# Kernel tuning notes

Measured on AMD Instinct MI355X. Metric: run time of the kernel, lower is better.

Reference implementation:

```python
import jax, jax.numpy as jnp
import numpy as np

HEADS = 4
KS = 7  # neighborhood window size


def group_norm(x, g, b, eps=1e-5):
    # GroupNorm(1, C) on NCHW: normalize over (C,H,W) per sample
    mu = x.mean(axis=(1, 2, 3), keepdims=True)
    var = x.var(axis=(1, 2, 3), keepdims=True)
    xn = (x - mu) * jax.lax.rsqrt(var + eps)
    return xn * g[None, :, None, None] + b[None, :, None, None]


def layer_norm(x, g, b, eps=1e-5):
    mu = x.mean(axis=-1, keepdims=True)
    var = x.var(axis=-1, keepdims=True)
    return (x - mu) * jax.lax.rsqrt(var + eps) * g + b


def na2d(x, qkv_w, qkv_b, proj_w, proj_b, rpb):
    # Neighborhood attention 2D (NATTEN semantics: window clamped at borders)
    N, H, W, C = x.shape
    e, k = HEADS, KS
    d = C // e
    qkv = x @ qkv_w.T + qkv_b  # [N,H,W,3C]
    q, kk, v = jnp.split(qkv, 3, axis=-1)
    q = q.reshape(N, H, W, e, d) * (d ** -0.5)
    kk = kk.reshape(N, H, W, e, d)
    v = v.reshape(N, H, W, e, d)
    ni = jnp.clip(jnp.arange(H) - k // 2, 0, H - k)[:, None] + jnp.arange(k)  # [H,k]
    nj = jnp.clip(jnp.arange(W) - k // 2, 0, W - k)[:, None] + jnp.arange(k)  # [W,k]
    kg = kk[:, ni][:, :, :, nj]  # [N,H,i,W,j,e,d]
    vg = v[:, ni][:, :, :, nj]
    scores = jnp.einsum('nhwed,nhiwjed->nhweij', q, kg)  # [N,H,W,e,k,k]
    ri = ni - jnp.arange(H)[:, None] + (k - 1)  # rel pos index in [0, 2k-2]
    rj = nj - jnp.arange(W)[:, None] + (k - 1)
    bias = rpb[:, ri][:, :, :, rj]  # [e,H,i,W,j]
    scores = scores + bias.transpose(1, 3, 0, 2, 4)[None]
    attn = jax.nn.softmax(scores.reshape(N, H, W, e, k * k), axis=-1).reshape(N, H, W, e, k, k)
    out = jnp.einsum('nhweij,nhiwjed->nhwed', attn, vg).reshape(N, H, W, C)
    return out @ proj_w.T + proj_b


def na_layer(x, gn_g, gn_b, qkv_w, qkv_b, proj_w, proj_b, rpb, ln_g, ln_b, fc1_w, fc1_b, fc2_w, fc2_b):
    N, C, H, W = x.shape
    x1 = x.transpose(0, 2, 3, 1)  # n h w c (pre-norm residual)
    xg = group_norm(x, gn_g, gn_b).transpose(0, 2, 3, 1)
    a = na2d(xg, qkv_w, qkv_b, proj_w, proj_b, rpb) + x1
    t = a.reshape(N, H * W, C)
    h = jax.nn.gelu(layer_norm(t, ln_g, ln_b) @ fc1_w.T + fc1_b, approximate=False)
    t = t + (h @ fc2_w.T + fc2_b)
    return t.reshape(N, H, W, C).transpose(0, 3, 1, 2)


def conv3x3(x, w, b):
    y = jax.lax.conv_general_dilated(x, w, (1, 1), 'SAME', dimension_numbers=('NCHW', 'OIHW', 'NCHW'))
    return y + b[None, :, None, None]


def setup_inputs() -> dict:
    key = jax.random.key(0)
    ks = jax.random.split(key, 16)
    N, C, H, W = 2, 128, 64, 64
    L, e, k, hid, red = 2, HEADS, KS, 4 * 128, 18
    rn = lambda kk, shape, s=0.02: jax.random.normal(kk, shape, jnp.float32) * s
    return {
        'x': jax.random.normal(ks[0], (N, C, H, W), jnp.float32),
        'gn_g': jnp.ones((L, C), jnp.float32), 'gn_b': jnp.zeros((L, C), jnp.float32),
        'qkv_w': rn(ks[1], (L, 3 * C, C)), 'qkv_b': jnp.zeros((L, 3 * C), jnp.float32),
        'proj_w': rn(ks[2], (L, C, C)), 'proj_b': jnp.zeros((L, C), jnp.float32),
        'rpb': rn(ks[3], (L, e, 2 * k - 1, 2 * k - 1)),
        'ln_g': jnp.ones((L, C), jnp.float32), 'ln_b': jnp.zeros((L, C), jnp.float32),
        'fc1_w': rn(ks[4], (L, hid, C)), 'fc1_b': jnp.zeros((L, hid), jnp.float32),
        'fc2_w': rn(ks[5], (L, C, hid)), 'fc2_b': jnp.zeros((L, C), jnp.float32),
        'bconv_w': rn(ks[6], (C, C, 3, 3)), 'bconv_b': jnp.zeros((C,), jnp.float32),
        'c1_w': rn(ks[7], (C // 4, C)), 'c1_b': jnp.zeros((C // 4,), jnp.float32),
        'c2_w': rn(ks[8], (C, C // 4)), 'c2_b': jnp.zeros((C,), jnp.float32),
        'ca1_w': rn(ks[9], (C // red, C)), 'ca1_b': jnp.zeros((C // red,), jnp.float32),
        'ca2_w': rn(ks[10], (C, C // red)), 'ca2_b': jnp.zeros((C,), jnp.float32),
    }


def reference(x, gn_g, gn_b, qkv_w, qkv_b, proj_w, proj_b, rpb, ln_g, ln_b, fc1_w, fc1_b, fc2_w, fc2_b, bconv_w, bconv_b, c1_w, c1_b, c2_w, c2_b, ca1_w, ca1_b, ca2_w, ca2_b):
    res = x
    for l in range(gn_g.shape[0]):  # n_resblocks (structurally fixed, small)
        res = na_layer(res, gn_g[l], gn_b[l], qkv_w[l], qkv_b[l], proj_w[l], proj_b[l], rpb[l],
                       ln_g[l], ln_b[l], fc1_w[l], fc1_b[l], fc2_w[l], fc2_b[l])
    res = conv3x3(res, bconv_w, bconv_b)
    # tail: 1x1 conv -> ReLU -> 1x1 conv -> CALayer
    y = jax.nn.relu(jnp.einsum('rc,nchw->nrhw', c1_w, res) + c1_b[None, :, None, None])
    y = jnp.einsum('cr,nrhw->nchw', c2_w, y) + c2_b[None, :, None, None]
    p = y.mean(axis=(2, 3))  # global avg pool -> [N,C]
    s = jax.nn.sigmoid(jax.nn.relu(p @ ca1_w.T + ca1_b) @ ca2_w.T + ca2_b)
    y = y * s[:, :, None, None]
    return y + x
```

## Files before the change

### kernel.cpp

```cpp
#include <hip/hip_runtime.h>
#include <math.h>

typedef unsigned short u16;

#define NN 2
#define CC 128
#define HH 64
#define WW 64
#define NHD 4
#define DH 32
#define KSZ 7
#define NB 49
#define PIX (NN*HH*WW)
#define HID 512
#define C4 32
#define CRED 7
#define RW 22
#define RNB 160
#define NBV 154

typedef float f32x4 __attribute__((ext_vector_type(4)));
typedef short bf16x8 __attribute__((ext_vector_type(8)));

static __device__ __forceinline__ float u2f(u16 u){ return __uint_as_float(((unsigned)u) << 16); }
static __device__ __forceinline__ u16 f2u(float f){
    unsigned b = __float_as_uint(f);
    return (u16)((b + 0x7FFFu + ((b >> 16) & 1u)) >> 16);
}

__global__ void detect_k(const u16* __restrict__ x, int* __restrict__ flag,
                         float* __restrict__ poolacc){
    __shared__ float red[256];
    int t = threadIdx.x;
    float mx = 0.f;
    for(int i = t; i < 4096; i += 256){
        float v = fabsf(u2f(x[i]));
        if(v < 1e30f) mx = fmaxf(mx, v);
    }
    red[t] = mx; __syncthreads();
    for(int s = 128; s > 0; s >>= 1){
        if(t < s) red[t] = fmaxf(red[t], red[t+s]);
        __syncthreads();
    }
    if(t == 0) *flag = (red[0] > 1e6f) ? 1 : 0;
    if(t < NN*CC) poolacc[t] = 0.f;
}

struct PtrTab { const void* p[23]; int off[24]; };

__global__ void cvt_all_k(PtrTab tab, u16* __restrict__ dst, const int* __restrict__ flag, int total){
    int i = blockIdx.x*256 + threadIdx.x;
    if(i >= total) return;
    int a = 0;
    while(i >= tab.off[a+1]) a++;
    int loc = i - tab.off[a];
    dst[i] = (*flag) ? f2u(((const float*)tab.p[a])[loc]) : ((const u16*)tab.p[a])[loc];
}

__global__ void repack_conv_k(const u16* __restrict__ src, u16* __restrict__ dst){
    int i = blockIdx.x*256 + threadIdx.x;
    if(i >= CC*CC*9) return;
    int o = i/(9*CC); int rem = i%(9*CC); int tap = rem/CC; int c = rem%CC;
    dst[i] = src[(o*CC + c)*9 + tap];
}

__global__ __launch_bounds__(256) void nchw_k(const void* __restrict__ x, float* __restrict__ cur,
                                              float* __restrict__ part, const int* __restrict__ flag){
    __shared__ float tile[32][65];
    __shared__ float wred[4][2];
    int bx = blockIdx.x;
    int by = blockIdx.y;
    int n = by >> 6, i = by & 63;
    int t = threadIdx.x;
    int fl = *flag;
    for(int idx = t; idx < 32*64; idx += 256){
        int cl = idx >> 6, j = idx & 63;
        size_t src = ((size_t)(n*CC + bx*32 + cl)*HH + i)*WW + j;
        tile[cl][j] = fl ? ((const float*)x)[src] : u2f(((const u16*)x)[src]);
    }
    __syncthreads();
    float s = 0.f, q = 0.f;
    for(int idx = t; idx < 64*32; idx += 256){
        int j = idx >> 5, cl = idx & 31;
        float v = tile[cl][j];
        cur[((size_t)((n*HH + i)*WW) + j)*CC + bx*32 + cl] = v;
        s += v; q += v*v;
    }
    #pragma unroll
    for(int off = 32; off > 0; off >>= 1){ s += __shfl_xor(s, off, 64); q += __shfl_xor(q, off, 64); }
    int wave = t >> 6;
    if((t & 63) == 0){ wred[wave][0] = s; wred[wave][1] = q; }
    __syncthreads();
    if(t == 0){
        float ss = wred[0][0]+wred[1][0]+wred[2][0]+wred[3][0];
        float qq = wred[0][1]+wred[1][1]+wred[2][1]+wred[3][1];
        int pidx = n*256 + (by & 63)*4 + bx;
        part[pidx*2] = ss; part[pidx*2+1] = qq;
    }
}

__global__ void gn_r2_k(const float* __restrict__ part, float* __restrict__ stats, int count){
    __shared__ float s1[256]; __shared__ float s2[256];
    int n = blockIdx.x, t = threadIdx.x;
    float a = 0.f, q = 0.f;
    for(int idx = t; idx < count; idx += 256){
        a += part[(n*count + idx)*2];
        q += part[(n*count + idx)*2 + 1];
    }
    s1[t] = a; s2[t] = q; __syncthreads();
    for(int s = 128; s > 0; s >>= 1){
        if(t < s){ s1[t] += s1[t+s]; s2[t] += s2[t+s]; }
        __syncthreads();
    }
    if(t == 0){
        const float inv = 1.f/(float)(HH*WW*CC);
        float mu = s1[0]*inv;
        float var = fmaxf(s2[0]*inv - mu*mu, 0.f);
        stats[n*2] = mu; stats[n*2+1] = rsqrtf(var + 1e-5f);
    }
}

enum { EPI_NONE = 0, EPI_RES = 1, EPI_GELU = 2, EPI_RELU = 3 };
enum { OUT_F32 = 0, OUT_BF16 = 1, OUT_BOTH = 2 };
enum { EX_NONE = 0, EX_STATS = 1, EX_POOL = 2 };

template<int BK, int EPI, int OUTM, int AGN, int EXTRA>
__global__ __launch_bounds__(256) void g64_k(
    const void* __restrict__ Av, const u16* __restrict__ W, const u16* __restrict__ bias,
    const float* __restrict__ R, float* __restrict__ Cf, u16* __restrict__ Cb,
    const float* __restrict__ stats, const u16* __restrict__ gnw, const u16* __restrict__ gnb,
    float* __restrict__ gnpart, float* __restrict__ poolacc,
    int M, int N, int K)
{
    const int LDP = BK + 8;
    const int CH  = BK/8;
    const int NL  = (64*CH)/256;
    __shared__ __align__(16) u16 As[64*(BK+8)];
    __shared__ __align__(16) u16 Bs[64*(BK+8)];
    __shared__ float wred[4][2];
    const int bm = blockIdx.y*64, bn = blockIdx.x*64;
    const int t = threadIdx.x;
    const int wave = t >> 6, lane = t & 63;
    const int wm = (wave >> 1)*32, wn = (wave & 1)*32;
    const int lg = lane >> 4, lr = lane & 15;
    const int nsm = bm >> 12;
    f32x4 acc[2][2];
    #pragma unroll
    for(int i = 0; i < 2; i++)
        #pragma unroll
        for(int j = 0; j < 2; j++) acc[i][j] = (f32x4){0.f,0.f,0.f,0.f};

    float gmu = 0.f, grs = 0.f;
    if(AGN){ gmu = stats[nsm*2]; grs = stats[nsm*2+1]; }

    for(int k0 = 0; k0 < K; k0 += BK){
        uint4 ra[NL], rb[NL];
        float4 fa[NL][2];
        #pragma unroll
        for(int r = 0; r < NL; r++){
            int e = r*256 + t;
            int row = e / CH, ch = e % CH;
            if(AGN){
                const float* ap = (const float*)Av + (size_t)(bm+row)*K + k0 + ch*8;
                fa[r][0] = *(const float4*)ap;
                fa[r][1] = *(const float4*)(ap + 4);
            } else {
                ra[r] = *(const uint4*)((const u16*)Av + (size_t)(bm+row)*K + k0 + ch*8);
            }
            rb[r] = (bn+row < N) ? *(const uint4*)(W + (size_t)(bn+row)*K + k0 + ch*8)
                                 : (uint4){0,0,0,0};
        }
        #pragma unroll
        for(int r = 0; r < NL; r++){
            int e = r*256 + t;
            int row = e / CH, ch = e % CH;
            if(AGN){
                union { uint4 u; u16 h[8]; } g8, b8, o8;
                g8.u = *(const uint4*)(gnw + k0 + ch*8);
                b8.u = *(const uint4*)(gnb + k0 + ch*8);
                const float* fv = (const float*)&fa[r][0];
                #pragma unroll
                for(int z = 0; z < 8; z++)
                    o8.h[z] = f2u((fv[z]-gmu)*grs*u2f(g8.h[z]) + u2f(b8.h[z]));
                *(uint4*)&As[row*LDP + ch*8] = o8.u;
            } else {
                *(uint4*)&As[row*LDP + ch*8] = ra[r];
            }
            *(uint4*)&Bs[row*LDP + ch*8] = rb[r];
        }
        __syncthreads();
        #pragma unroll
        for(int kc = 0; kc < BK/32; kc++){
            bf16x8 af0 = *(const bf16x8*)&As[(wm + lr)*LDP      + kc*32 + lg*8];
            bf16x8 af1 = *(const bf16x8*)&As[(wm + 16 + lr)*LDP + kc*32 + lg*8];
            bf16x8 bf0 = *(const bf16x8*)&Bs[(wn + lr)*LDP      + kc*32 + lg*8];
            bf16x8 bf1 = *(const bf16x8*)&Bs[(wn + 16 + lr)*LDP + kc*32 + lg*8];
            acc[0][0] = __builtin_amdgcn_mfma_f32_16x16x32_bf16(af0, bf0, acc[0][0], 0, 0, 0);
            acc[0][1] = __builtin_amdgcn_mfma_f32_16x16x32_bf16(af0, bf1, acc[0][1], 0, 0, 0);
            acc[1][0] = __builtin_amdgcn_mfma_f32_16x16x32_bf16(af1, bf0, acc[1][0], 0, 0, 0);
            acc[1][1] = __builtin_amdgcn_mfma_f32_16x16x32_bf16(af1, bf1, acc[1][1], 0, 0, 0);
        }
        __syncthreads();
    }

    float ssum = 0.f, sq = 0.f;
    float cs[2] = {0.f, 0.f};
    #pragma unroll
    for(int i = 0; i < 2; i++){
        #pragma unroll
        for(int j = 0; j < 2; j++){
            int col = bn + wn + j*16 + lr;
            if(col >= N) continue;
            #pragma unroll
            for(int reg = 0; reg < 4; reg++){
                int row = bm + wm + i*16 + lg*4 + reg;
                float v = acc[i][j][reg] + u2f(bias[col]);
                if(EPI == EPI_RES)  v += R[(size_t)row*N + col];
                if(EPI == EPI_GELU) v = 0.5f*v*(1.f + erff(v*0.70710678118f));
                if(EPI == EPI_RELU) v = fmaxf(v, 0.f);
                if(OUTM == OUT_F32 || OUTM == OUT_BOTH) Cf[(size_t)row*N + col] = v;
                if(OUTM == OUT_BF16 || OUTM == OUT_BOTH) Cb[(size_t)row*N + col] = f2u(v);
                if(EXTRA == EX_STATS){ ssum += v; sq += v*v; }
                if(EXTRA == EX_POOL) cs[j] += v;
            }
        }
    }
    if(EXTRA == EX_STATS){
        #pragma unroll
        for(int off = 32; off > 0; off >>= 1){
            ssum += __shfl_xor(ssum, off, 64); sq += __shfl_xor(sq, off, 64);
        }
        if(lane == 0){ wred[wave][0] = ssum; wred[wave][1] = sq; }
        __syncthreads();
        if(t == 0){
            int bidx = blockIdx.y*gridDim.x + blockIdx.x;
            gnpart[bidx*2]   = wred[0][0]+wred[1][0]+wred[2][0]+wred[3][0];
            gnpart[bidx*2+1] = wred[0][1]+wred[1][1]+wred[2][1]+wred[3][1];
        }
    }
    if(EXTRA == EX_POOL){
        #pragma unroll
        for(int j = 0; j < 2; j++){
            cs[j] += __shfl_xor(cs[j], 16, 64);
            cs[j] += __shfl_xor(cs[j], 32, 64);
        }
        if(lg == 0){
            #pragma unroll
            for(int j = 0; j < 2; j++){
                int col = bn + wn + j*16 + lr;
                if(col < N) atomicAdd(&poolacc[nsm*CC + col], cs[j]);
            }
        }
    }
}

__global__ __launch_bounds__(256) void mconv_k(
    const u16* __restrict__ in, const u16* __restrict__ Wt,
    const u16* __restrict__ bias, u16* __restrict__ Cb)
{
    const int LDP = 72;
    __shared__ __align__(16) u16 As[64*72];
    __shared__ __align__(16) u16 Bs[64*72];
    const int bm = blockIdx.y*64, bn = blockIdx.x*64;
    const int t = threadIdx.x;
    const int wave = t >> 6, lane = t & 63;
    const int wm = (wave >> 1)*32, wn = (wave & 1)*32;
    const int lg = lane >> 4, lr = lane & 15;
    f32x4 acc[2][2];
    #pragma unroll
    for(int i = 0; i < 2; i++)
        #pragma unroll
        for(int j = 0; j < 2; j++) acc[i][j] = (f32x4){0.f,0.f,0.f,0.f};

    for(int k0 = 0; k0 < 9*CC; k0 += 64){
        int tap = k0 >> 7; int dy = tap/3 - 1, dx = tap%3 - 1;
        int coff = k0 & 127;
        uint4 ra[2], rb[2];
        #pragma unroll
        for(int r = 0; r < 2; r++){
            int e = r*256 + t;
            int row = e >> 3, ch = e & 7;
            int p = bm + row;
            int n = p >> 12, ii = (p & 4095) >> 6, jj = p & 63;
            int y = ii + dy, x = jj + dx;
            ra[r] = (uint4){0,0,0,0};
            if(y >= 0 && y < HH && x >= 0 && x < WW)
                ra[r] = *(const uint4*)(in + (size_t)(((n*HH + y)*WW + x))*CC + coff + ch*8);
            rb[r] = *(const uint4*)(Wt + (size_t)(bn+row)*(9*CC) + k0 + ch*8);
        }
        #pragma unroll
        for(int r = 0; r < 2; r++){
            int e = r*256 + t;
            int row = e >> 3, ch = e & 7;
            *(uint4*)&As[row*LDP + ch*8] = ra[r];
            *(uint4*)&Bs[row*LDP + ch*8] = rb[r];
        }
        __syncthreads();
        #pragma unroll
        for(int kc = 0; kc < 2; kc++){
            bf16x8 af0 = *(const bf16x8*)&As[(wm + lr)*LDP      + kc*32 + lg*8];
            bf16x8 af1 = *(const bf16x8*)&As[(wm + 16 + lr)*LDP + kc*32 + lg*8];
            bf16x8 bf0 = *(const bf16x8*)&Bs[(wn + lr)*LDP      + kc*32 + lg*8];
            bf16x8 bf1 = *(const bf16x8*)&Bs[(wn + 16 + lr)*LDP + kc*32 + lg*8];
            acc[0][0] = __builtin_amdgcn_mfma_f32_16x16x32_bf16(af0, bf0, acc[0][0], 0, 0, 0);
            acc[0][1] = __builtin_amdgcn_mfma_f32_16x16x32_bf16(af0, bf1, acc[0][1], 0, 0, 0);
            acc[1][0] = __builtin_amdgcn_mfma_f32_16x16x32_bf16(af1, bf0, acc[1][0], 0, 0, 0);
            acc[1][1] = __builtin_amdgcn_mfma_f32_16x16x32_bf16(af1, bf1, acc[1][1], 0, 0, 0);
        }
        __syncthreads();
    }
    #pragma unroll
    for(int i = 0; i < 2; i++){
        #pragma unroll
        for(int j = 0; j < 2; j++){
            int col = bn + wn + j*16 + lr;
            #pragma unroll
            for(int reg = 0; reg < 4; reg++){
                int row = bm + wm + i*16 + lg*4 + reg;
                Cb[(size_t)row*CC + col] = f2u(acc[i][j][reg] + u2f(bias[col]));
            }
        }
    }
}

#define KVP 72
#define PSP 168

__global__ __launch_bounds__(128) void att_tile_k(
    const u16* __restrict__ qkv, const u16* __restrict__ rpb, u16* __restrict__ out)
{
    __shared__ __align__(16) u16 KV[2][RNB][KVP];
    __shared__ __align__(16) u16 Qs[16][64];
    __shared__ __align__(16) u16 Ps[2][16][PSP];
    __shared__ float rpbs[2][169];
    const int blk = blockIdx.x;
    const int rb = blk >> 1, eg = blk & 1;
    const int p0 = rb*16;
    const int jb = p0 & 63, i = (p0 >> 6) & 63, n = p0 >> 12;
    const int i0 = min(max(i-3, 0), HH-KSZ);
    const int rc0 = min(max(jb-3, 0), WW-KSZ);
    const int t = threadIdx.x;

    for(int idx = t; idx < 2*169; idx += 128)
        rpbs[idx/169][idx%169] = u2f(rpb[(eg*2 + idx/169)*169 + idx%169]);
    {
        int pix = t >> 3, ch = t & 7;
        *(uint4*)&Qs[pix][ch*8] = *(const uint4*)(qkv + (size_t)(p0+pix)*(3*CC) + eg*64 + ch*8);
    }
    for(int idx = t; idx < RNB*16; idx += 128){
        int nb = idx >> 4, part = idx & 15;
        int kv = part >> 3, ch = part & 7;
        uint4 v = (uint4){0,0,0,0};
        if(nb < NBV){
            int ky = nb/RW, kcol = nb - ky*RW;
            int sy = i0 + ky, sx = min(rc0 + kcol, WW-1);
            v = *(const uint4*)(qkv + (size_t)((n*HH + sy)*WW + sx)*(3*CC) + CC + kv*CC + eg*64 + ch*8);
        }
        *(uint4*)&KV[kv][nb][ch*8] = v;
    }
    __syncthreads();

    const int el = t >> 6;
    const int lane = t & 63, lg = lane >> 4, lr = lane & 15;

    bf16x8 aq = *(const bf16x8*)&Qs[lr][el*32 + lg*8];
    f32x4 sc[10];
    #pragma unroll
    for(int c = 0; c < 10; c++){
        bf16x8 bk = *(const bf16x8*)&KV[0][c*16+lr][el*32 + lg*8];
        sc[c] = __builtin_amdgcn_mfma_f32_16x16x32_bf16(aq, bk, (f32x4){0.f,0.f,0.f,0.f}, 0, 0, 0);
    }
    #pragma unroll
    for(int reg = 0; reg < 4; reg++){
        int pix = lg*4 + reg;
        int j = jb + pix;
        int base = min(max(j-3, 0), WW-KSZ) - rc0;
        float mx = -1e30f;
        #pragma unroll
        for(int c = 0; c < 10; c++){
            int nb = c*16 + lr;
            int ky = nb/RW, kcol = nb - ky*RW;
            float v = -1e30f;
            if(nb < NBV && kcol >= base && kcol <= base+6){
                int ri = i0 + ky - i + (KSZ-1);
                int rj = rc0 + kcol - j + (KSZ-1);
                v = sc[c][reg]*0.17677669529663689f + rpbs[el][ri*13 + rj];
            }
            sc[c][reg] = v;
            mx = fmaxf(mx, v);
        }
        mx = fmaxf(mx, __shfl_xor(mx, 1, 64));
        mx = fmaxf(mx, __shfl_xor(mx, 2, 64));
        mx = fmaxf(mx, __shfl_xor(mx, 4, 64));
        mx = fmaxf(mx, __shfl_xor(mx, 8, 64));
        float sum = 0.f;
        #pragma unroll
        for(int c = 0; c < 10; c++){
            float p = __expf(sc[c][reg] - mx);
            sc[c][reg] = p; sum += p;
        }
        sum += __shfl_xor(sum, 1, 64);
        sum += __shfl_xor(sum, 2, 64);
        sum += __shfl_xor(sum, 4, 64);
        sum += __shfl_xor(sum, 8, 64);
        float rs = 1.f/sum;
        #pragma unroll
        for(int c = 0; c < 10; c++)
            Ps[el][pix][c*16+lr] = f2u(sc[c][reg]*rs);
    }
    __syncthreads();
    f32x4 o0 = (f32x4){0.f,0.f,0.f,0.f}, o1 = (f32x4){0.f,0.f,0.f,0.f};
    #pragma unroll
    for(int ks = 0; ks < 5; ks++){
        bf16x8 ap = *(const bf16x8*)&Ps[el][lr][ks*32 + lg*8];
        bf16x8 b0, b1;
        #pragma unroll
        for(int jj = 0; jj < 8; jj++){
            int nb = ks*32 + lg*8 + jj;
            b0[jj] = (short)KV[1][nb][el*32 + lr];
            b1[jj] = (short)KV[1][nb][el*32 + 16 + lr];
        }
        o0 = __builtin_amdgcn_mfma_f32_16x16x32_bf16(ap, b0, o0, 0, 0, 0);
        o1 = __builtin_amdgcn_mfma_f32_16x16x32_bf16(ap, b1, o1, 0, 0, 0);
    }
    int e = eg*2 + el;
    #pragma unroll
    for(int reg = 0; reg < 4; reg++){
        int pix = lg*4 + reg;
        out[(size_t)(p0+pix)*CC + e*32 + lr]      = f2u(o0[reg]);
        out[(size_t)(p0+pix)*CC + e*32 + 16 + lr] = f2u(o1[reg]);
    }
}

__global__ void ln_k(const float* __restrict__ a, const u16* __restrict__ g,
                     const u16* __restrict__ b, u16* __restrict__ out){
    int wave = threadIdx.x >> 6;
    int lane = threadIdx.x & 63;
    int p = blockIdx.x*4 + wave;
    if(p >= PIX) return;
    const float* row = a + (size_t)p*CC;
    float v1 = row[lane], v2 = row[lane+64];
    float s = v1 + v2, q = v1*v1 + v2*v2;
    #pragma unroll
    for(int off = 32; off > 0; off >>= 1){
        s += __shfl_xor(s, off, 64);
        q += __shfl_xor(q, off, 64);
    }
    float mu = s*(1.f/CC);
    float rstd = rsqrtf(fmaxf(q*(1.f/CC) - mu*mu, 0.f) + 1e-5f);
    u16* o = out + (size_t)p*CC;
    o[lane]    = f2u((v1-mu)*rstd*u2f(g[lane])    + u2f(b[lane]));
    o[lane+64] = f2u((v2-mu)*rstd*u2f(g[lane+64]) + u2f(b[lane+64]));
}

__global__ void ca_k(const float* __restrict__ poolacc,
                     const u16* __restrict__ w1, const u16* __restrict__ b1,
                     const u16* __restrict__ w2, const u16* __restrict__ b2,
                     float* __restrict__ s){
    __shared__ float pl[CC]; __shared__ float t1[CRED];
    int n = blockIdx.x, t = threadIdx.x;
    pl[t] = poolacc[n*CC + t]*(1.f/(HH*WW));
    __syncthreads();
    if(t < CRED){
        float a = u2f(b1[t]);
        for(int c = 0; c < CC; c++) a += pl[c]*u2f(w1[t*CC + c]);
        t1[t] = fmaxf(a, 0.f);
    }
    __syncthreads();
    float a = u2f(b2[t]);
    #pragma unroll
    for(int r = 0; r < CRED; r++) a += t1[r]*u2f(w2[t*CRED + r]);
    s[n*CC + t] = 1.f/(1.f + __expf(-a));
}

__global__ void final_k(const float* __restrict__ y, const float* __restrict__ s,
                        const void* __restrict__ xraw, void* __restrict__ outv,
                        const int* __restrict__ flag){
    int id = blockIdx.x*256 + threadIdx.x;
    if(id >= NN*CC*HH*WW) return;
    int j = id % WW; int i = (id/WW) % HH; int c = (id/(WW*HH)) % CC; int n = id/(WW*HH*CC);
    float xr = (*flag) ? ((const float*)xraw)[id] : u2f(((const u16*)xraw)[id]);
    float v = y[(size_t)((n*HH + i)*WW + j)*CC + c]*s[n*CC + c] + xr;
    if(*flag) ((float*)outv)[id] = v;
    else      ((u16*)outv)[id] = f2u(v);
}

extern "C" void kernel_launch(void* const* d_in, const int* in_sizes, int n_in,
                              void* d_out, int out_size, void* d_ws, size_t ws_size,
                              hipStream_t stream){
    float* wsf    = (float*)d_ws;
    int*   flagp  = (int*)d_ws;
    float* stats  = wsf + 4;
    float* gnpart = wsf + 8;
    float* poolacc= wsf + 1040;
    float* sbuf   = wsf + 1300;

    u16* Wb = (u16*)(wsf + 2048);
    static const int wsizes[23] = {256,256,98304,768,32768,256,1352,256,256,131072,1024,
                                   131072,256,147456,128,4096,32,4096,128,896,7,896,128};
    int woff[24]; woff[0] = 0;
    for(int i = 0; i < 23; i++) woff[i+1] = woff[i] + wsizes[i];
    const int WTOT = woff[23];
    u16* Wt = Wb + 555760;

    float* AB    = wsf + 360448;
    float* cur   = AB;
    u16*  cur16  = (u16*)(AB + 1048576);
    u16*  xg16   = (u16*)(AB + 1572864);
    u16*  qkv16  = (u16*)(AB + 2097152);
    float* abuf  = AB + 2097152;
    u16*  hbuf16 = (u16*)(AB + 3670016);
    float* ybuf  = AB + 3670016;
    u16*  y1     = (u16*)(AB + 4718592);

    detect_k<<<1, 256, 0, stream>>>((const u16*)d_in[0], flagp, poolacc);

    PtrTab tab;
    for(int i = 0; i < 23; i++){ tab.p[i] = d_in[i+1]; tab.off[i] = woff[i]; }
    tab.off[23] = woff[23];
    cvt_all_k<<<(WTOT + 255)/256, 256, 0, stream>>>(tab, Wb, flagp, WTOT);
    repack_conv_k<<<(CC*CC*9 + 255)/256, 256, 0, stream>>>(Wb + woff[13], Wt);

    const u16 *gng = Wb+woff[0], *gnb = Wb+woff[1], *qkvw = Wb+woff[2], *qkvb = Wb+woff[3],
              *projw = Wb+woff[4], *projb = Wb+woff[5], *rpbw = Wb+woff[6], *lng = Wb+woff[7],
              *lnb = Wb+woff[8], *f1w = Wb+woff[9], *f1b = Wb+woff[10], *f2w = Wb+woff[11],
              *f2b = Wb+woff[12], *bcb = Wb+woff[14], *c1w = Wb+woff[15],
              *c1b = Wb+woff[16], *c2w = Wb+woff[17], *c2b = Wb+woff[18], *ca1w = Wb+woff[19],
              *ca1b = Wb+woff[20], *ca2w = Wb+woff[21], *ca2b = Wb+woff[22];

    nchw_k<<<dim3(4, NN*HH), 256, 0, stream>>>(d_in[0], cur, gnpart, flagp);

    for(int l = 0; l < 2; l++){
        gn_r2_k<<<NN, 256, 0, stream>>>(gnpart, stats, l == 0 ? 256 : 128);

        g64_k<64,EPI_NONE,OUT_BF16,1,EX_NONE><<<dim3(6, PIX/64), 256, 0, stream>>>(
            cur, qkvw + (size_t)l*3*CC*CC, qkvb + l*3*CC, nullptr, nullptr, qkv16,
            stats, gng + l*CC, gnb + l*CC, nullptr, nullptr, PIX, 3*CC, CC);

        att_tile_k<<<PIX/16*2, 128, 0, stream>>>(qkv16, rpbw + l*NHD*169, xg16);

        g64_k<64,EPI_RES,OUT_F32,0,EX_NONE><<<dim3(2, PIX/64), 256, 0, stream>>>(
            xg16, projw + (size_t)l*CC*CC, projb + l*CC, cur, abuf, nullptr,
            nullptr, nullptr, nullptr, nullptr, nullptr, PIX, CC, CC);

        ln_k<<<PIX/4, 256, 0, stream>>>(abuf, lng + l*CC, lnb + l*CC, xg16);

        g64_k<64,EPI_GELU,OUT_BF16,0,EX_NONE><<<dim3(8, PIX/64), 256, 0, stream>>>(
            xg16, f1w + (size_t)l*HID*CC, f1b + l*HID, nullptr, nullptr, hbuf16,
            nullptr, nullptr, nullptr, nullptr, nullptr, PIX, HID, CC);

        g64_k<64,EPI_RES,OUT_BOTH,0,EX_STATS><<<dim3(2, PIX/64), 256, 0, stream>>>(
            hbuf16, f2w + (size_t)l*CC*HID, f2b + l*CC, abuf, cur, cur16,
            nullptr, nullptr, nullptr, gnpart, nullptr, PIX, CC, HID);
    }

    mconv_k<<<dim3(2, PIX/64), 256, 0, stream>>>(cur16, Wt, bcb, xg16);

    g64_k<64,EPI_RELU,OUT_BF16,0,EX_NONE><<<dim3(1, PIX/64), 256, 0, stream>>>(
        xg16, c1w, c1b, nullptr, nullptr, y1,
        nullptr, nullptr, nullptr, nullptr, nullptr, PIX, C4, CC);

    g64_k<32,EPI_NONE,OUT_F32,0,EX_POOL><<<dim3(2, PIX/64), 256, 0, stream>>>(
        y1, c2w, c2b, nullptr, ybuf, nullptr,
        nullptr, nullptr, nullptr, nullptr, poolacc, PIX, CC, C4);

    ca_k<<<NN, CC, 0, stream>>>(poolacc, ca1w, ca1b, ca2w, ca2b, sbuf);
    final_k<<<(NN*CC*HH*WW)/256, 256, 0, stream>>>(ybuf, sbuf, d_in[0], d_out, flagp);
}
```

Baseline: 298.6 us.

## Fuse setup, GN stats, proj+LayerNorm, tail GEMMs and CA into fewer kernels

```diff
diff --git a/kernel.cpp b/kernel.cpp
--- a/kernel.cpp
+++ b/kernel.cpp
@@ -10,7 +10,6 @@
 #define NHD 4
 #define DH 32
 #define KSZ 7
-#define NB 49
 #define PIX (NN*HH*WW)
 #define HID 512
 #define C4 32
@@ -47,32 +46,43 @@
 }
 
 struct PtrTab { const void* p[23]; int off[24]; };
-
-__global__ void cvt_all_k(PtrTab tab, u16* __restrict__ dst, const int* __restrict__ flag, int total){
-    int i = blockIdx.x*256 + threadIdx.x;
-    if(i >= total) return;
-    int a = 0;
-    while(i >= tab.off[a+1]) a++;
-    int loc = i - tab.off[a];
-    dst[i] = (*flag) ? f2u(((const float*)tab.p[a])[loc]) : ((const u16*)tab.p[a])[loc];
-}
-
-__global__ void repack_conv_k(const u16* __restrict__ src, u16* __restrict__ dst){
-    int i = blockIdx.x*256 + threadIdx.x;
-    if(i >= CC*CC*9) return;
-    int o = i/(9*CC); int rem = i%(9*CC); int tap = rem/CC; int c = rem%CC;
-    dst[i] = src[(o*CC + c)*9 + tap];
-}
-
-__global__ __launch_bounds__(256) void nchw_k(const void* __restrict__ x, float* __restrict__ cur,
-                                              float* __restrict__ part, const int* __restrict__ flag){
+#define NCVT 2172
+#define NRPK 576
+#define NNCH 512
+
+__global__ __launch_bounds__(256) void setup_k(
+    PtrTab tab, u16* __restrict__ Wb, u16* __restrict__ Wt,
+    const void* __restrict__ convw, const void* __restrict__ x,
+    float* __restrict__ cur, float* __restrict__ part,
+    const int* __restrict__ flag, int total)
+{
+    int blk = blockIdx.x;
+    int t = threadIdx.x;
+    int fl = *flag;
+    if(blk < NCVT){
+        int i = blk*256 + t;
+        if(i < total){
+            int a = 0;
+            while(i >= tab.off[a+1]) a++;
+            int loc = i - tab.off[a];
+            Wb[i] = fl ? f2u(((const float*)tab.p[a])[loc]) : ((const u16*)tab.p[a])[loc];
+        }
+        return;
+    }
+    if(blk < NCVT + NRPK){
+        int i = (blk - NCVT)*256 + t;
+        if(i < CC*CC*9){
+            int o = i/(9*CC); int rem = i%(9*CC); int tap = rem/CC; int c = rem%CC;
+            size_t s = (size_t)(o*CC + c)*9 + tap;
+            Wt[i] = fl ? f2u(((const float*)convw)[s]) : ((const u16*)convw)[s];
+        }
+        return;
+    }
     __shared__ float tile[32][65];
     __shared__ float wred[4][2];
-    int bx = blockIdx.x;
-    int by = blockIdx.y;
+    int u = blk - NCVT - NRPK;
+    int bx = u & 3, by = u >> 2;
     int n = by >> 6, i = by & 63;
-    int t = threadIdx.x;
-    int fl = *flag;
     for(int idx = t; idx < 32*64; idx += 256){
         int cl = idx >> 6, j = idx & 63;
         size_t src = ((size_t)(n*CC + bx*32 + cl)*HH + i)*WW + j;
@@ -94,49 +104,26 @@
     if(t == 0){
         float ss = wred[0][0]+wred[1][0]+wred[2][0]+wred[3][0];
         float qq = wred[0][1]+wred[1][1]+wred[2][1]+wred[3][1];
-        int pidx = n*256 + (by & 63)*4 + bx;
+        int pidx = n*256 + i*4 + bx;
         part[pidx*2] = ss; part[pidx*2+1] = qq;
     }
 }
 
-__global__ void gn_r2_k(const float* __restrict__ part, float* __restrict__ stats, int count){
-    __shared__ float s1[256]; __shared__ float s2[256];
-    int n = blockIdx.x, t = threadIdx.x;
-    float a = 0.f, q = 0.f;
-    for(int idx = t; idx < count; idx += 256){
-        a += part[(n*count + idx)*2];
-        q += part[(n*count + idx)*2 + 1];
-    }
-    s1[t] = a; s2[t] = q; __syncthreads();
-    for(int s = 128; s > 0; s >>= 1){
-        if(t < s){ s1[t] += s1[t+s]; s2[t] += s2[t+s]; }
-        __syncthreads();
-    }
-    if(t == 0){
-        const float inv = 1.f/(float)(HH*WW*CC);
-        float mu = s1[0]*inv;
-        float var = fmaxf(s2[0]*inv - mu*mu, 0.f);
-        stats[n*2] = mu; stats[n*2+1] = rsqrtf(var + 1e-5f);
-    }
-}
-
-enum { EPI_NONE = 0, EPI_RES = 1, EPI_GELU = 2, EPI_RELU = 3 };
+enum { EPI_NONE = 0, EPI_RES = 1, EPI_GELU = 2 };
 enum { OUT_F32 = 0, OUT_BF16 = 1, OUT_BOTH = 2 };
-enum { EX_NONE = 0, EX_STATS = 1, EX_POOL = 2 };
-
-template<int BK, int EPI, int OUTM, int AGN, int EXTRA>
+enum { EX_NONE = 0, EX_STATS = 1 };
+#define LDP 136
+
+template<int EPI, int OUTM, int AGN, int EXTRA>
 __global__ __launch_bounds__(256) void g64_k(
     const void* __restrict__ Av, const u16* __restrict__ W, const u16* __restrict__ bias,
     const float* __restrict__ R, float* __restrict__ Cf, u16* __restrict__ Cb,
-    const float* __restrict__ stats, const u16* __restrict__ gnw, const u16* __restrict__ gnb,
-    float* __restrict__ gnpart, float* __restrict__ poolacc,
+    const u16* __restrict__ gnw, const u16* __restrict__ gnb,
+    float* __restrict__ gnpart, int gncount,
     int M, int N, int K)
 {
-    const int LDP = BK + 8;
-    const int CH  = BK/8;
-    const int NL  = (64*CH)/256;
-    __shared__ __align__(16) u16 As[64*(BK+8)];
-    __shared__ __align__(16) u16 Bs[64*(BK+8)];
+    __shared__ __align__(16) u16 As[64*LDP];
+    __shared__ __align__(16) u16 Bs[64*LDP];
     __shared__ float wred[4][2];
     const int bm = blockIdx.y*64, bn = blockIdx.x*64;
     const int t = threadIdx.x;
@@ -151,15 +138,28 @@
         for(int j = 0; j < 2; j++) acc[i][j] = (f32x4){0.f,0.f,0.f,0.f};
 
     float gmu = 0.f, grs = 0.f;
-    if(AGN){ gmu = stats[nsm*2]; grs = stats[nsm*2+1]; }
-
-    for(int k0 = 0; k0 < K; k0 += BK){
-        uint4 ra[NL], rb[NL];
-        float4 fa[NL][2];
-        #pragma unroll
-        for(int r = 0; r < NL; r++){
+    if(AGN){
+        float a = 0.f, q = 0.f;
+        for(int idx = lane; idx < gncount; idx += 64){
+            a += gnpart[(nsm*gncount + idx)*2];
+            q += gnpart[(nsm*gncount + idx)*2 + 1];
+        }
+        #pragma unroll
+        for(int off = 32; off > 0; off >>= 1){
+            a += __shfl_xor(a, off, 64); q += __shfl_xor(q, off, 64);
+        }
+        const float inv = 1.f/(float)(HH*WW*CC);
+        gmu = a*inv;
+        grs = rsqrtf(fmaxf(q*inv - gmu*gmu, 0.f) + 1e-5f);
+    }
+
+    for(int k0 = 0; k0 < K; k0 += 128){
+        uint4 ra[4], rb[4];
+        float4 fa[4][2];
+        #pragma unroll
+        for(int r = 0; r < 4; r++){
             int e = r*256 + t;
-            int row = e / CH, ch = e % CH;
+            int row = e >> 4, ch = e & 15;
             if(AGN){
                 const float* ap = (const float*)Av + (size_t)(bm+row)*K + k0 + ch*8;
                 fa[r][0] = *(const float4*)ap;
@@ -171,9 +171,9 @@
                                  : (uint4){0,0,0,0};
         }
         #pragma unroll
-        for(int r = 0; r < NL; r++){
+        for(int r = 0; r < 4; r++){
             int e = r*256 + t;
-            int row = e / CH, ch = e % CH;
+            int row = e >> 4, ch = e & 15;
             if(AGN){
                 union { uint4 u; u16 h[8]; } g8, b8, o8;
                 g8.u = *(const uint4*)(gnw + k0 + ch*8);
@@ -190,7 +190,7 @@
         }
         __syncthreads();
         #pragma unroll
-        for(int kc = 0; kc < BK/32; kc++){
+        for(int kc = 0; kc < 4; kc++){
             bf16x8 af0 = *(const bf16x8*)&As[(wm + lr)*LDP      + kc*32 + lg*8];
             bf16x8 af1 = *(const bf16x8*)&As[(wm + 16 + lr)*LDP + kc*32 + lg*8];
             bf16x8 bf0 = *(const bf16x8*)&Bs[(wn + lr)*LDP      + kc*32 + lg*8];
@@ -200,11 +200,10 @@
             acc[1][0] = __builtin_amdgcn_mfma_f32_16x16x32_bf16(af1, bf0, acc[1][0], 0, 0, 0);
             acc[1][1] = __builtin_amdgcn_mfma_f32_16x16x32_bf16(af1, bf1, acc[1][1], 0, 0, 0);
         }
-        __syncthreads();
+        if(k0 + 128 < K) __syncthreads();
     }
 
     float ssum = 0.f, sq = 0.f;
-    float cs[2] = {0.f, 0.f};
     #pragma unroll
     for(int i = 0; i < 2; i++){
         #pragma unroll
@@ -217,11 +216,9 @@
                 float v = acc[i][j][reg] + u2f(bias[col]);
                 if(EPI == EPI_RES)  v += R[(size_t)row*N + col];
                 if(EPI == EPI_GELU) v = 0.5f*v*(1.f + erff(v*0.70710678118f));
-                if(EPI == EPI_RELU) v = fmaxf(v, 0.f);
                 if(OUTM == OUT_F32 || OUTM == OUT_BOTH) Cf[(size_t)row*N + col] = v;
                 if(OUTM == OUT_BF16 || OUTM == OUT_BOTH) Cb[(size_t)row*N + col] = f2u(v);
                 if(EXTRA == EX_STATS){ ssum += v; sq += v*v; }
-                if(EXTRA == EX_POOL) cs[j] += v;
             }
         }
     }
@@ -238,17 +235,106 @@
             gnpart[bidx*2+1] = wred[0][1]+wred[1][1]+wred[2][1]+wred[3][1];
         }
     }
-    if(EXTRA == EX_POOL){
-        #pragma unroll
-        for(int j = 0; j < 2; j++){
-            cs[j] += __shfl_xor(cs[j], 16, 64);
-            cs[j] += __shfl_xor(cs[j], 32, 64);
-        }
-        if(lg == 0){
-            #pragma unroll
-            for(int j = 0; j < 2; j++){
-                int col = bn + wn + j*16 + lr;
-                if(col < N) atomicAdd(&poolacc[nsm*CC + col], cs[j]);
+}
+
+__global__ __launch_bounds__(256) void proj_ln_k(
+    const u16* __restrict__ A, const u16* __restrict__ W, const u16* __restrict__ bias,
+    const float* __restrict__ R, const u16* __restrict__ lng, const u16* __restrict__ lnb,
+    float* __restrict__ abuf, u16* __restrict__ lnout)
+{
+    __shared__ __align__(16) u16 As[64*LDP];
+    __shared__ __align__(16) u16 Bs[128*LDP];
+    __shared__ float redS[64][2], redQ[64][2], muS[64], rsS[64];
+    const int bm = blockIdx.x*64;
+    const int t = threadIdx.x;
+    const int wave = t >> 6, lane = t & 63;
+    const int wm = (wave >> 1)*32, wn = (wave & 1)*64;
+    const int lg = lane >> 4, lr = lane & 15;
+
+    {
+        uint4 ra[4], rb[8];
+        #pragma unroll
+        for(int r = 0; r < 4; r++){
+            int e = r*256 + t; int row = e >> 4, ch = e & 15;
+            ra[r] = *(const uint4*)(A + (size_t)(bm+row)*CC + ch*8);
+        }
+        #pragma unroll
+        for(int r = 0; r < 8; r++){
+            int e = r*256 + t; int row = e >> 4, ch = e & 15;
+            rb[r] = *(const uint4*)(W + (size_t)row*CC + ch*8);
+        }
+        #pragma unroll
+        for(int r = 0; r < 4; r++){
+            int e = r*256 + t; int row = e >> 4, ch = e & 15;
+            *(uint4*)&As[row*LDP + ch*8] = ra[r];
+        }
+        #pragma unroll
+        for(int r = 0; r < 8; r++){
+            int e = r*256 + t; int row = e >> 4, ch = e & 15;
+            *(uint4*)&Bs[row*LDP + ch*8] = rb[r];
+        }
+    }
+    __syncthreads();
+
+    f32x4 acc[2][4];
+    #pragma unroll
+    for(int i = 0; i < 2; i++)
+        #pragma unroll
+        for(int j = 0; j < 4; j++) acc[i][j] = (f32x4){0.f,0.f,0.f,0.f};
+    #pragma unroll
+    for(int kc = 0; kc < 4; kc++){
+        bf16x8 af[2], bf[4];
+        #pragma unroll
+        for(int i = 0; i < 2; i++)
+            af[i] = *(const bf16x8*)&As[(wm + i*16 + lr)*LDP + kc*32 + lg*8];
+        #pragma unroll
+        for(int j = 0; j < 4; j++)
+            bf[j] = *(const bf16x8*)&Bs[(wn + j*16 + lr)*LDP + kc*32 + lg*8];
+        #pragma unroll
+        for(int i = 0; i < 2; i++)
+            #pragma unroll
+            for(int j = 0; j < 4; j++)
+                acc[i][j] = __builtin_amdgcn_mfma_f32_16x16x32_bf16(af[i], bf[j], acc[i][j], 0, 0, 0);
+    }
+    #pragma unroll
+    for(int i = 0; i < 2; i++){
+        #pragma unroll
+        for(int reg = 0; reg < 4; reg++){
+            int rl = wm + i*16 + lg*4 + reg;
+            float rs_ = 0.f, rq_ = 0.f;
+            #pragma unroll
+            for(int j = 0; j < 4; j++){
+                int col = wn + j*16 + lr;
+                float v = acc[i][j][reg] + u2f(bias[col]) + R[(size_t)(bm+rl)*CC + col];
+                acc[i][j][reg] = v;
+                abuf[(size_t)(bm+rl)*CC + col] = v;
+                rs_ += v; rq_ += v*v;
+            }
+            rs_ += __shfl_xor(rs_, 1, 64); rq_ += __shfl_xor(rq_, 1, 64);
+            rs_ += __shfl_xor(rs_, 2, 64); rq_ += __shfl_xor(rq_, 2, 64);
+            rs_ += __shfl_xor(rs_, 4, 64); rq_ += __shfl_xor(rq_, 4, 64);
+            rs_ += __shfl_xor(rs_, 8, 64); rq_ += __shfl_xor(rq_, 8, 64);
+            if(lr == 0){ redS[rl][wn>>6] = rs_; redQ[rl][wn>>6] = rq_; }
+        }
+    }
+    __syncthreads();
+    if(t < 64){
+        float mu = (redS[t][0] + redS[t][1])*(1.f/CC);
+        float var = fmaxf((redQ[t][0] + redQ[t][1])*(1.f/CC) - mu*mu, 0.f);
+        muS[t] = mu; rsS[t] = rsqrtf(var + 1e-5f);
+    }
+    __syncthreads();
+    #pragma unroll
+    for(int i = 0; i < 2; i++){
+        #pragma unroll
+        for(int reg = 0; reg < 4; reg++){
+            int rl = wm + i*16 + lg*4 + reg;
+            float mu = muS[rl], rstd = rsS[rl];
+            #pragma unroll
+            for(int j = 0; j < 4; j++){
+                int col = wn + j*16 + lr;
+                float v = (acc[i][j][reg] - mu)*rstd*u2f(lng[col]) + u2f(lnb[col]);
+                lnout[(size_t)(bm+rl)*CC + col] = f2u(v);
             }
         }
     }
@@ -258,9 +344,8 @@
     const u16* __restrict__ in, const u16* __restrict__ Wt,
     const u16* __restrict__ bias, u16* __restrict__ Cb)
 {
-    const int LDP = 72;
-    __shared__ __align__(16) u16 As[64*72];
-    __shared__ __align__(16) u16 Bs[64*72];
+    __shared__ __align__(16) u16 As[64*LDP];
+    __shared__ __align__(16) u16 Bs[64*LDP];
     const int bm = blockIdx.y*64, bn = blockIdx.x*64;
     const int t = threadIdx.x;
     const int wave = t >> 6, lane = t & 63;
@@ -272,32 +357,32 @@
         #pragma unroll
         for(int j = 0; j < 2; j++) acc[i][j] = (f32x4){0.f,0.f,0.f,0.f};
 
-    for(int k0 = 0; k0 < 9*CC; k0 += 64){
-        int tap = k0 >> 7; int dy = tap/3 - 1, dx = tap%3 - 1;
-        int coff = k0 & 127;
-        uint4 ra[2], rb[2];
-        #pragma unroll
-        for(int r = 0; r < 2; r++){
+    for(int tap = 0; tap < 9; tap++){
+        int dy = tap/3 - 1, dx = tap%3 - 1;
+        int k0 = tap*128;
+        uint4 ra[4], rb[4];
+        #pragma unroll
+        for(int r = 0; r < 4; r++){
             int e = r*256 + t;
-            int row = e >> 3, ch = e & 7;
+            int row = e >> 4, ch = e & 15;
             int p = bm + row;
             int n = p >> 12, ii = (p & 4095) >> 6, jj = p & 63;
             int y = ii + dy, x = jj + dx;
             ra[r] = (uint4){0,0,0,0};
             if(y >= 0 && y < HH && x >= 0 && x < WW)
-                ra[r] = *(const uint4*)(in + (size_t)(((n*HH + y)*WW + x))*CC + coff + ch*8);
+                ra[r] = *(const uint4*)(in + (size_t)(((n*HH + y)*WW + x))*CC + ch*8);
             rb[r] = *(const uint4*)(Wt + (size_t)(bn+row)*(9*CC) + k0 + ch*8);
         }
         #pragma unroll
-        for(int r = 0; r < 2; r++){
+        for(int r = 0; r < 4; r++){
             int e = r*256 + t;
-            int row = e >> 3, ch = e & 7;
+            int row = e >> 4, ch = e & 15;
             *(uint4*)&As[row*LDP + ch*8] = ra[r];
             *(uint4*)&Bs[row*LDP + ch*8] = rb[r];
         }
         __syncthreads();
         #pragma unroll
-        for(int kc = 0; kc < 2; kc++){
+        for(int kc = 0; kc < 4; kc++){
             bf16x8 af0 = *(const bf16x8*)&As[(wm + lr)*LDP      + kc*32 + lg*8];
             bf16x8 af1 = *(const bf16x8*)&As[(wm + 16 + lr)*LDP + kc*32 + lg*8];
             bf16x8 bf0 = *(const bf16x8*)&Bs[(wn + lr)*LDP      + kc*32 + lg*8];
@@ -307,7 +392,7 @@
             acc[1][0] = __builtin_amdgcn_mfma_f32_16x16x32_bf16(af1, bf0, acc[1][0], 0, 0, 0);
             acc[1][1] = __builtin_amdgcn_mfma_f32_16x16x32_bf16(af1, bf1, acc[1][1], 0, 0, 0);
         }
-        __syncthreads();
+        if(tap < 8) __syncthreads();
     }
     #pragma unroll
     for(int i = 0; i < 2; i++){
@@ -432,55 +517,158 @@
     }
 }
 
-__global__ void ln_k(const float* __restrict__ a, const u16* __restrict__ g,
-                     const u16* __restrict__ b, u16* __restrict__ out){
-    int wave = threadIdx.x >> 6;
-    int lane = threadIdx.x & 63;
-    int p = blockIdx.x*4 + wave;
-    if(p >= PIX) return;
-    const float* row = a + (size_t)p*CC;
-    float v1 = row[lane], v2 = row[lane+64];
-    float s = v1 + v2, q = v1*v1 + v2*v2;
-    #pragma unroll
-    for(int off = 32; off > 0; off >>= 1){
-        s += __shfl_xor(s, off, 64);
-        q += __shfl_xor(q, off, 64);
-    }
-    float mu = s*(1.f/CC);
-    float rstd = rsqrtf(fmaxf(q*(1.f/CC) - mu*mu, 0.f) + 1e-5f);
-    u16* o = out + (size_t)p*CC;
-    o[lane]    = f2u((v1-mu)*rstd*u2f(g[lane])    + u2f(b[lane]));
-    o[lane+64] = f2u((v2-mu)*rstd*u2f(g[lane+64]) + u2f(b[lane+64]));
-}
-
-__global__ void ca_k(const float* __restrict__ poolacc,
-                     const u16* __restrict__ w1, const u16* __restrict__ b1,
-                     const u16* __restrict__ w2, const u16* __restrict__ b2,
-                     float* __restrict__ s){
-    __shared__ float pl[CC]; __shared__ float t1[CRED];
-    int n = blockIdx.x, t = threadIdx.x;
-    pl[t] = poolacc[n*CC + t]*(1.f/(HH*WW));
-    __syncthreads();
+__global__ __launch_bounds__(256) void tail_k(
+    const u16* __restrict__ A, const u16* __restrict__ c1w, const u16* __restrict__ c1b,
+    const u16* __restrict__ c2w, const u16* __restrict__ c2b,
+    float* __restrict__ ybuf, float* __restrict__ poolacc)
+{
+    __shared__ __align__(16) u16 As[64*LDP];
+    __shared__ __align__(16) u16 Bs1[32*LDP];
+    __shared__ __align__(16) u16 Hs[64*40];
+    __shared__ __align__(16) u16 Bs2[128*40];
+    const int bm = blockIdx.x*64;
+    const int t = threadIdx.x;
+    const int wave = t >> 6, lane = t & 63;
+    const int lg = lane >> 4, lr = lane & 15;
+    const int nsm = bm >> 12;
+
+    {
+        uint4 ra[4], rb1[2], rb2[2];
+        #pragma unroll
+        for(int r = 0; r < 4; r++){
+            int e = r*256 + t; int row = e >> 4, ch = e & 15;
+            ra[r] = *(const uint4*)(A + (size_t)(bm+row)*CC + ch*8);
+        }
+        #pragma unroll
+        for(int r = 0; r < 2; r++){
+            int e = r*256 + t; int row = e >> 4, ch = e & 15;
+            rb1[r] = *(const uint4*)(c1w + (size_t)row*CC + ch*8);
+        }
+        #pragma unroll
+        for(int r = 0; r < 2; r++){
+            int e = r*256 + t; int row = e >> 2, ch = e & 3;
+            rb2[r] = *(const uint4*)(c2w + (size_t)row*C4 + ch*8);
+        }
+        #pragma unroll
+        for(int r = 0; r < 4; r++){
+            int e = r*256 + t; int row = e >> 4, ch = e & 15;
+            *(uint4*)&As[row*LDP + ch*8] = ra[r];
+        }
+        #pragma unroll
+        for(int r = 0; r < 2; r++){
+            int e = r*256 + t; int row = e >> 4, ch = e & 15;
+            *(uint4*)&Bs1[row*LDP + ch*8] = rb1[r];
+        }
+        #pragma unroll
+        for(int r = 0; r < 2; r++){
+            int e = r*256 + t; int row = e >> 2, ch = e & 3;
+            *(uint4*)&Bs2[row*40 + ch*8] = rb2[r];
+        }
+    }
+    __syncthreads();
+
+    {
+        const int wm1 = (wave >> 1)*32, wn1 = (wave & 1)*16;
+        f32x4 a1[2];
+        a1[0] = (f32x4){0.f,0.f,0.f,0.f}; a1[1] = (f32x4){0.f,0.f,0.f,0.f};
+        #pragma unroll
+        for(int kc = 0; kc < 4; kc++){
+            bf16x8 bf = *(const bf16x8*)&Bs1[(wn1 + lr)*LDP + kc*32 + lg*8];
+            bf16x8 af0 = *(const bf16x8*)&As[(wm1 + lr)*LDP      + kc*32 + lg*8];
+            bf16x8 af1 = *(const bf16x8*)&As[(wm1 + 16 + lr)*LDP + kc*32 + lg*8];
+            a1[0] = __builtin_amdgcn_mfma_f32_16x16x32_bf16(af0, bf, a1[0], 0, 0, 0);
+            a1[1] = __builtin_amdgcn_mfma_f32_16x16x32_bf16(af1, bf, a1[1], 0, 0, 0);
+        }
+        #pragma unroll
+        for(int i = 0; i < 2; i++){
+            #pragma unroll
+            for(int reg = 0; reg < 4; reg++){
+                int rl = wm1 + i*16 + lg*4 + reg;
+                int col = wn1 + lr;
+                Hs[rl*40 + col] = f2u(fmaxf(a1[i][reg] + u2f(c1b[col]), 0.f));
+            }
+        }
+    }
+    __syncthreads();
+
+    {
+        const int wm = (wave >> 1)*32, wn = (wave & 1)*64;
+        f32x4 a2[2][4];
+        #pragma unroll
+        for(int i = 0; i < 2; i++)
+            #pragma unroll
+            for(int j = 0; j < 4; j++) a2[i][j] = (f32x4){0.f,0.f,0.f,0.f};
+        bf16x8 af[2];
+        #pragma unroll
+        for(int i = 0; i < 2; i++)
+            af[i] = *(const bf16x8*)&Hs[(wm + i*16 + lr)*40 + lg*8];
+        #pragma unroll
+        for(int j = 0; j < 4; j++){
+            bf16x8 bf = *(const bf16x8*)&Bs2[(wn + j*16 + lr)*40 + lg*8];
+            a2[0][j] = __builtin_amdgcn_mfma_f32_16x16x32_bf16(af[0], bf, a2[0][j], 0, 0, 0);
+            a2[1][j] = __builtin_amdgcn_mfma_f32_16x16x32_bf16(af[1], bf, a2[1][j], 0, 0, 0);
+        }
+        float cs[4] = {0.f,0.f,0.f,0.f};
+        #pragma unroll
+        for(int i = 0; i < 2; i++){
+            #pragma unroll
+            for(int j = 0; j < 4; j++){
+                int col = wn + j*16 + lr;
+                #pragma unroll
+                for(int reg = 0; reg < 4; reg++){
+                    int row = bm + wm + i*16 + lg*4 + reg;
+                    float v = a2[i][j][reg] + u2f(c2b[col]);
+                    ybuf[(size_t)row*CC + col] = v;
+                    cs[j] += v;
+                }
+            }
+        }
+        #pragma unroll
+        for(int j = 0; j < 4; j++){
+            cs[j] += __shfl_xor(cs[j], 16, 64);
+            cs[j] += __shfl_xor(cs[j], 32, 64);
+        }
+        if(lg == 0){
+            #pragma unroll
+            for(int j = 0; j < 4; j++)
+                atomicAdd(&poolacc[nsm*CC + wn + j*16 + lr], cs[j]);
+        }
+    }
+}
+
+__global__ __launch_bounds__(256) void final_ca_k(
+    const float* __restrict__ y, const float* __restrict__ poolacc,
+    const u16* __restrict__ w1, const u16* __restrict__ b1,
+    const u16* __restrict__ w2, const u16* __restrict__ b2,
+    const void* __restrict__ xraw, void* __restrict__ outv,
+    const int* __restrict__ flag)
+{
+    __shared__ float t1s[CRED];
+    __shared__ float sres;
+    int id0 = blockIdx.x*256;
+    int c = (id0 >> 12) & (CC-1);
+    int n = id0 >> 19;
+    int t = threadIdx.x;
     if(t < CRED){
         float a = u2f(b1[t]);
-        for(int c = 0; c < CC; c++) a += pl[c]*u2f(w1[t*CC + c]);
-        t1[t] = fmaxf(a, 0.f);
-    }
-    __syncthreads();
-    float a = u2f(b2[t]);
-    #pragma unroll
-    for(int r = 0; r < CRED; r++) a += t1[r]*u2f(w2[t*CRED + r]);
-    s[n*CC + t] = 1.f/(1.f + __expf(-a));
-}
-
-__global__ void final_k(const float* __restrict__ y, const float* __restrict__ s,
-                        const void* __restrict__ xraw, void* __restrict__ outv,
-                        const int* __restrict__ flag){
-    int id = blockIdx.x*256 + threadIdx.x;
-    if(id >= NN*CC*HH*WW) return;
-    int j = id % WW; int i = (id/WW) % HH; int c = (id/(WW*HH)) % CC; int n = id/(WW*HH*CC);
+        const float pscale = 1.f/(float)(HH*WW);
+        for(int cc = 0; cc < CC; cc++)
+            a += poolacc[n*CC + cc]*pscale*u2f(w1[t*CC + cc]);
+        t1s[t] = fmaxf(a, 0.f);
+    }
+    __syncthreads();
+    if(t == 0){
+        float a = u2f(b2[c]);
+        #pragma unroll
+        for(int r = 0; r < CRED; r++) a += t1s[r]*u2f(w2[c*CRED + r]);
+        sres = 1.f/(1.f + __expf(-a));
+    }
+    __syncthreads();
+    float s = sres;
+    int id = id0 + t;
+    int j = id & 63; int i = (id >> 6) & 63;
     float xr = (*flag) ? ((const float*)xraw)[id] : u2f(((const u16*)xraw)[id]);
-    float v = y[(size_t)((n*HH + i)*WW + j)*CC + c]*s[n*CC + c] + xr;
+    float v = y[(size_t)((n*HH + i)*WW + j)*CC + c]*s + xr;
     if(*flag) ((float*)outv)[id] = v;
     else      ((u16*)outv)[id] = f2u(v);
 }
@@ -490,10 +678,8 @@
                               hipStream_t stream){
     float* wsf    = (float*)d_ws;
     int*   flagp  = (int*)d_ws;
-    float* stats  = wsf + 4;
     float* gnpart = wsf + 8;
     float* poolacc= wsf + 1040;
-    float* sbuf   = wsf + 1300;
 
     u16* Wb = (u16*)(wsf + 2048);
     static const int wsizes[23] = {256,256,98304,768,32768,256,1352,256,256,131072,1024,
@@ -511,15 +697,14 @@
     float* abuf  = AB + 2097152;
     u16*  hbuf16 = (u16*)(AB + 3670016);
     float* ybuf  = AB + 3670016;
-    u16*  y1     = (u16*)(AB + 4718592);
 
     detect_k<<<1, 256, 0, stream>>>((const u16*)d_in[0], flagp, poolacc);
 
     PtrTab tab;
     for(int i = 0; i < 23; i++){ tab.p[i] = d_in[i+1]; tab.off[i] = woff[i]; }
     tab.off[23] = woff[23];
-    cvt_all_k<<<(WTOT + 255)/256, 256, 0, stream>>>(tab, Wb, flagp, WTOT);
-    repack_conv_k<<<(CC*CC*9 + 255)/256, 256, 0, stream>>>(Wb + woff[13], Wt);
+    setup_k<<<NCVT + NRPK + NNCH, 256, 0, stream>>>(
+        tab, Wb, Wt, d_in[14], d_in[0], cur, gnpart, flagp, WTOT);
 
     const u16 *gng = Wb+woff[0], *gnb = Wb+woff[1], *qkvw = Wb+woff[2], *qkvb = Wb+woff[3],
               *projw = Wb+woff[4], *projb = Wb+woff[5], *rpbw = Wb+woff[6], *lng = Wb+woff[7],
@@ -528,42 +713,32 @@
               *c1b = Wb+woff[16], *c2w = Wb+woff[17], *c2b = Wb+woff[18], *ca1w = Wb+woff[19],
               *ca1b = Wb+woff[20], *ca2w = Wb+woff[21], *ca2b = Wb+woff[22];
 
-    nchw_k<<<dim3(4, NN*HH), 256, 0, stream>>>(d_in[0], cur, gnpart, flagp);
-
     for(int l = 0; l < 2; l++){
-        gn_r2_k<<<NN, 256, 0, stream>>>(gnpart, stats, l == 0 ? 256 : 128);
-
-        g64_k<64,EPI_NONE,OUT_BF16,1,EX_NONE><<<dim3(6, PIX/64), 256, 0, stream>>>(
+        int gncount = (l == 0) ? 256 : 128;
+
+        g64_k<EPI_NONE,OUT_BF16,1,EX_NONE><<<dim3(6, PIX/64), 256, 0, stream>>>(
             cur, qkvw + (size_t)l*3*CC*CC, qkvb + l*3*CC, nullptr, nullptr, qkv16,
-            stats, gng + l*CC, gnb + l*CC, nullptr, nullptr, PIX, 3*CC, CC);
+            gng + l*CC, gnb + l*CC, gnpart, gncount, PIX, 3*CC, CC);
 
         att_tile_k<<<PIX/16*2, 128, 0, stream>>>(qkv16, rpbw + l*NHD*169, xg16);
 
-        g64_k<64,EPI_RES,OUT_F32,0,EX_NONE><<<dim3(2, PIX/64), 256, 0, stream>>>(
-            xg16, projw + (size_t)l*CC*CC, projb + l*CC, cur, abuf, nullptr,
-            nullptr, nullptr, nullptr, nullptr, nullptr, PIX, CC, CC);
-
-        ln_k<<<PIX/4, 256, 0, stream>>>(abuf, lng + l*CC, lnb + l*CC, xg16);
-
-        g64_k<64,EPI_GELU,OUT_BF16,0,EX_NONE><<<dim3(8, PIX/64), 256, 0, stream>>>(
+        proj_ln_k<<<PIX/64, 256, 0, stream>>>(
+            xg16, projw + (size_t)l*CC*CC, projb + l*CC, cur, lng + l*CC, lnb + l*CC,
+            abuf, xg16);
+
+        g64_k<EPI_GELU,OUT_BF16,0,EX_NONE><<<dim3(8, PIX/64), 256, 0, stream>>>(
             xg16, f1w + (size_t)l*HID*CC, f1b + l*HID, nullptr, nullptr, hbuf16,
-            nullptr, nullptr, nullptr, nullptr, nullptr, PIX, HID, CC);
-
-        g64_k<64,EPI_RES,OUT_BOTH,0,EX_STATS><<<dim3(2, PIX/64), 256, 0, stream>>>(
+            nullptr, nullptr, nullptr, 0, PIX, HID, CC);
+
+        g64_k<EPI_RES,OUT_BOTH,0,EX_STATS><<<dim3(2, PIX/64), 256, 0, stream>>>(
             hbuf16, f2w + (size_t)l*CC*HID, f2b + l*CC, abuf, cur, cur16,
-            nullptr, nullptr, nullptr, gnpart, nullptr, PIX, CC, HID);
+            nullptr, nullptr, gnpart, 0, PIX, CC, HID);
     }
 
     mconv_k<<<dim3(2, PIX/64), 256, 0, stream>>>(cur16, Wt, bcb, xg16);
 
-    g64_k<64,EPI_RELU,OUT_BF16,0,EX_NONE><<<dim3(1, PIX/64), 256, 0, stream>>>(
-        xg16, c1w, c1b, nullptr, nullptr, y1,
-        nullptr, nullptr, nullptr, nullptr, nullptr, PIX, C4, CC);
-
-    g64_k<32,EPI_NONE,OUT_F32,0,EX_POOL><<<dim3(2, PIX/64), 256, 0, stream>>>(
-        y1, c2w, c2b, nullptr, ybuf, nullptr,
-        nullptr, nullptr, nullptr, nullptr, poolacc, PIX, CC, C4);
-
-    ca_k<<<NN, CC, 0, stream>>>(poolacc, ca1w, ca1b, ca2w, ca2b, sbuf);
-    final_k<<<(NN*CC*HH*WW)/256, 256, 0, stream>>>(ybuf, sbuf, d_in[0], d_out, flagp);
-}
+    tail_k<<<PIX/64, 256, 0, stream>>>(xg16, c1w, c1b, c2w, c2b, ybuf, poolacc);
+
+    final_ca_k<<<(NN*CC*HH*WW)/256, 256, 0, stream>>>(
+        ybuf, poolacc, ca1w, ca1b, ca2w, ca2b, d_in[0], d_out, flagp);
+}
```

Result: faster. 268.9 us (-10.0%).
